# Performance work log

Measured on AMD Instinct MI355X. Metric: run time of the kernel, lower is better.

## Reference

```python
import jax, jax.numpy as jnp
import numpy as np

EPS = 1e-15


def _cdist(a, b):
    # batched euclidean pairwise distance, a:[B,N,K] b:[B,M,K] -> [B,N,M]
    d2 = (jnp.sum(a * a, -1)[:, :, None] + jnp.sum(b * b, -1)[:, None, :]
          - 2.0 * jnp.einsum('bik,bjk->bij', a, b))
    return jnp.sqrt(jnp.maximum(d2, 0.0))


def _rank3_diag(d_flat):
    # [B,N] -> [B,N,N] diagonal
    eye = jnp.eye(d_flat.shape[1], dtype=d_flat.dtype)
    return eye * d_flat[:, :, None]


def _trace(m):
    return jnp.einsum('bjj->b', m)


def dense_ct_rewiring(x, adj, s, mask):
    s = jnp.tanh(s)
    m = mask[:, :, None].astype(x.dtype)
    x = x * m
    s = s * m
    k = s.shape[-1]
    d_flat = jnp.sum(adj, axis=-1)              # [B,N]
    d = _rank3_diag(d_flat) + EPS               # EPS added to full matrix (faithful to torch)
    L = d - adj
    out_adj = jnp.einsum('bnk,bnm,bml->bkl', s, L, s)
    ct_num = _trace(out_adj)
    ct_den = _trace(jnp.einsum('bnk,bnm,bml->bkl', s, d, s)) + EPS
    ct_dist = _cdist(s, s)                      # [B,N,N]
    vol = _trace(d)                             # [B]
    ct_dist = ct_dist / vol[:, None, None]
    adj_new = ct_dist * adj
    ct_loss = jnp.mean(ct_num / ct_den)
    ss = jnp.einsum('bnk,bnl->bkl', s, s)
    i_s = jnp.eye(k, dtype=ss.dtype)
    ss_n = jnp.sqrt(jnp.sum(ss * ss, axis=(-1, -2), keepdims=True))
    diff = ss / ss_n - i_s
    ortho_loss = jnp.sqrt(jnp.sum(diff * diff))  # global Frobenius norm, mean of scalar
    return adj_new, ct_loss, ortho_loss


def dense_mincut_pool(x, adj, s, mask):
    s = jax.nn.softmax(s, axis=-1)
    m = mask[:, :, None].astype(x.dtype)
    x = x * m
    s = s * m
    k = s.shape[-1]
    out = jnp.einsum('bnk,bnf->bkf', s, x)
    out_adj = jnp.einsum('bnk,bnm,bml->bkl', s, adj, s)
    mincut_num = _trace(out_adj)
    d_flat = jnp.sum(adj, axis=-1) + EPS
    d = _rank3_diag(d_flat)
    mincut_den = _trace(jnp.einsum('bnk,bnm,bml->bkl', s, d, s))
    mincut_loss = jnp.mean(-(mincut_num / mincut_den))
    ss = jnp.einsum('bnk,bnl->bkl', s, s)
    i_s = jnp.eye(k, dtype=ss.dtype)
    ss_n = jnp.sqrt(jnp.sum(ss * ss, axis=(-1, -2), keepdims=True))
    diff = ss / ss_n - i_s / jnp.sqrt(jnp.asarray(float(k), ss.dtype))
    ortho_loss = jnp.mean(jnp.sqrt(jnp.sum(diff * diff, axis=(-1, -2))))
    # zero diagonal, then symmetric degree normalization
    out_adj = out_adj * (1.0 - i_s)
    dk = jnp.sqrt(jnp.sum(out_adj, axis=-1) + EPS) + EPS  # [B,k]
    out_adj = out_adj / dk[:, None, :] / dk[:, :, None]
    return out, out_adj, mincut_loss, ortho_loss


def dense_graph_conv(x, adj, w_rel, b_rel, w_root):
    # PyG DenseGraphConv(aggr='add'): lin_rel(adj @ x) + lin_root(x)
    return jnp.matmul(jnp.matmul(adj, x), w_rel) + b_rel + jnp.matmul(x, w_root)


def ctnet_forward(x, adj, mask,
                  W_lin1, b_lin1, W_pool1, b_pool1, W_pool2, b_pool2,
                  Wrel1, brel1, Wroot1, Wrel2, brel2, Wroot2,
                  W_lin2, b_lin2, W_lin3, b_lin3):
    x = jnp.matmul(x, W_lin1) + b_lin1
    s1 = jnp.matmul(x, W_pool1) + b_pool1
    adj, ct_loss, ortho1 = dense_ct_rewiring(x, adj, s1, mask)
    x = dense_graph_conv(x, adj, Wrel1, brel1, Wroot1)
    s2 = jnp.matmul(x, W_pool2) + b_pool2
    x, adj, mincut2, ortho2 = dense_mincut_pool(x, adj, s2, mask)
    x = dense_graph_conv(x, adj, Wrel2, brel2, Wroot2)
    x = jnp.sum(x, axis=1)
    x = jax.nn.relu(jnp.matmul(x, W_lin2) + b_lin2)
    x = jnp.matmul(x, W_lin3) + b_lin3
    return jax.nn.log_softmax(x, axis=-1), ct_loss + ortho1, mincut2 + ortho2


def _init_lin(key, fan_in, fan_out):
    k1, k2 = jax.random.split(key)
    lim = 1.0 / np.sqrt(fan_in)
    W = jax.random.uniform(k1, (fan_in, fan_out), jnp.float32, -lim, lim)
    b = jax.random.uniform(k2, (fan_out,), jnp.float32, -lim, lim)
    return W, b


def setup_inputs() -> dict:
    key = jax.random.key(0)
    ks = jax.random.split(key, 12)
    B, N, Fin, H, K, OUT, K2 = 16, 1024, 128, 32, 64, 10, 16
    x = jax.random.normal(ks[0], (B, N, Fin), jnp.float32)
    adj = jax.random.uniform(ks[1], (B, N, N), jnp.float32)
    mask = jnp.ones((B, N), jnp.bool_)
    W_lin1, b_lin1 = _init_lin(ks[2], Fin, H)
    W_pool1, b_pool1 = _init_lin(ks[3], H, K)
    W_pool2, b_pool2 = _init_lin(ks[4], H, K2)
    Wrel1, brel1 = _init_lin(ks[5], H, H)
    Wroot1, _ = _init_lin(ks[6], H, H)
    Wrel2, brel2 = _init_lin(ks[7], H, H)
    Wroot2, _ = _init_lin(ks[8], H, H)
    W_lin2, b_lin2 = _init_lin(ks[9], H, H)
    W_lin3, b_lin3 = _init_lin(ks[10], H, OUT)
    return dict(x=x, adj=adj, mask=mask,
                W_lin1=W_lin1, b_lin1=b_lin1, W_pool1=W_pool1, b_pool1=b_pool1,
                W_pool2=W_pool2, b_pool2=b_pool2,
                Wrel1=Wrel1, brel1=brel1, Wroot1=Wroot1,
                Wrel2=Wrel2, brel2=brel2, Wroot2=Wroot2,
                W_lin2=W_lin2, b_lin2=b_lin2, W_lin3=W_lin3, b_lin3=b_lin3)


def reference(x, adj, mask,
              W_lin1, b_lin1, W_pool1, b_pool1, W_pool2, b_pool2,
              Wrel1, brel1, Wroot1, Wrel2, brel2, Wroot2,
              W_lin2, b_lin2, W_lin3, b_lin3):
    return ctnet_forward(x, adj, mask,
                         W_lin1, b_lin1, W_pool1, b_pool1, W_pool2, b_pool2,
                         Wrel1, brel1, Wroot1, Wrel2, brel2, Wroot2,
                         W_lin2, b_lin2, W_lin3, b_lin3)
```

## Files before the change

### kernel.cpp

```cpp
#include <hip/hip_runtime.h>

typedef unsigned short u16;
typedef unsigned int   u32;
typedef __attribute__((ext_vector_type(8))) short bf16x8;
typedef __attribute__((ext_vector_type(4))) float f32x4;

#define EPSF 1e-15f

__device__ __forceinline__ float* accp(float* xb, int b, int a) {
    return xb + (size_t)(b*1024 + a/14)*128 + 114 + (a % 14);
}

__device__ __forceinline__ float bf2f(u16 u) {
    union { u32 i; float f; } v; v.i = ((u32)u) << 16; return v.f;
}
__device__ __forceinline__ u16 f2bf(float f) {
    union { u32 i; float f; } v; v.f = f;
    u32 r = v.i + 0x7fffu + ((v.i >> 16) & 1u);
    return (u16)(r >> 16);
}

__global__ __launch_bounds__(256) void k_a(float* xb,
        const float* __restrict__ W1, const float* __restrict__ b1,
        const float* __restrict__ Wp1, const float* __restrict__ bp1)
{
    __shared__ float W1s[128*32];
    __shared__ float Wp1s[32*64];
    __shared__ float xs[16][128];
    __shared__ float x1s[16][32];
    int tid = threadIdx.x;
    for (int i = tid; i < 1024; i += 256)
        *(float4*)&W1s[i*4] = *(const float4*)&W1[i*4];
    for (int i = tid; i < 512; i += 256)
        *(float4*)&Wp1s[i*4] = *(const float4*)&Wp1[i*4];
    int rbase = blockIdx.x*16;
    for (int e = tid; e < 512; e += 256) {
        int rr = e >> 5, c = e & 31;
        *(float4*)&xs[rr][c*4] = *(const float4*)&xb[(size_t)(rbase + rr)*128 + c*4];
    }
    __syncthreads();
    int w = tid >> 6, l = tid & 63;
    int col = l & 31, half = l >> 5;
    #pragma unroll
    for (int i = 0; i < 4; ++i) {
        int rr = w*4 + i;
        float* xr = xb + (size_t)(rbase + rr)*128;
        if (l == 33) xr[96] = 0.f;
        if (l < 15) xr[113 + l] = 0.f;
        float acc = half ? 0.f : b1[col];
        const float* xrow = &xs[rr][half*64];
        const float* wrow = &W1s[half*64*32 + col];
        for (int f = 0; f < 64; ++f) acc += xrow[f]*wrow[f*32];
        acc += __shfl_down(acc, 32);
        if (l < 32) x1s[rr][l] = acc;
    }
    __syncthreads();
    #pragma unroll
    for (int i = 0; i < 4; ++i) {
        int rr = w*4 + i;
        float* xr = xb + (size_t)(rbase + rr)*128;
        if (l < 32) xr[64 + l] = x1s[rr][l];
        float acc = bp1[l];
        for (int h = 0; h < 32; ++h) acc += x1s[rr][h]*Wp1s[h*64 + l];
        float sv = tanhf(acc);
        u32 me = (u32)f2bf(sv);
        u32 nb = __shfl_down(me, 1);
        if (!(l & 1)) ((u32*)xr)[l >> 1] = me | (nb << 16);
        float svr = bf2f((u16)me);
        float qv = svr*svr;
        for (int off = 32; off; off >>= 1) qv += __shfl_down(qv, off);
        if (l == 0) xr[112] = qv;
    }
}

__global__ __launch_bounds__(256, 5) void k_c(const float* __restrict__ adj, float* xb,
                                              u32* __restrict__ anb)
{
    __shared__ __align__(16) u16 BufA[64*72];
    __shared__ __align__(16) u16 BufB[2][64*72];
    __shared__ __align__(16) float qAs[64], qBs[2][64];
    __shared__ float pw[2][4];
    int tid = threadIdx.x;
    int tjq = blockIdx.x, ti = blockIdx.y, b = blockIdx.z;
    int w = tid >> 6, lane = tid & 63;
    int q = lane >> 4, c16 = lane & 15;
    int rloc = w*16 + c16;
    size_t rowg = (size_t)(b*1024 + ti*64 + rloc);
    float4 a4s[2][4];
    #pragma unroll
    for (int tt = 0; tt < 2; ++tt)
        #pragma unroll
        for (int t = 0; t < 4; ++t)
            a4s[tt][t] = *(const float4*)&adj[rowg*1024 + (tjq*2 + tt)*64 + t*16 + q*4];
    const u32* xu = (const u32*)xb;
    for (int e = tid; e < 512; e += 256) {
        int n = e >> 3, c = e & 7;
        *(float4*)&BufA[n*72 + c*8] = *(const float4*)&xu[(size_t)(b*1024 + ti*64 + n)*128 + c*4];
    }
    for (int e = tid; e < 1024; e += 256) {
        int n2 = e >> 3, c = e & 7;
        int tt = n2 >> 6, n = n2 & 63;
        *(float4*)&BufB[tt][n*72 + c*8] =
            *(const float4*)&xu[(size_t)(b*1024 + (tjq*2 + tt)*64 + n)*128 + c*4];
    }
    if (tid < 64) qAs[tid] = xb[(size_t)(b*1024 + ti*64 + tid)*128 + 112];
    else if (tid < 192) {
        int t2 = tid - 64;
        qBs[t2 >> 6][t2 & 63] =
            xb[(size_t)(b*1024 + (tjq*2 + (t2 >> 6))*64 + (t2 & 63))*128 + 112];
    }
    __syncthreads();
    bf16x8 bfr0 = *(const bf16x8*)&BufA[rloc*72 + q*8];
    bf16x8 bfr1 = *(const bf16x8*)&BufA[rloc*72 + 32 + q*8];
    float qa = qAs[rloc];
    float dsum = 0.f, rsum = 0.f, Pt = 0.f, Qt = 0.f;
    #pragma unroll
    for (int tt = 0; tt < 2; ++tt) {
        f32x4 g[4];
        #pragma unroll
        for (int t = 0; t < 4; ++t) {
            bf16x8 af0 = *(const bf16x8*)&BufB[tt][(t*16 + c16)*72 + q*8];
            bf16x8 af1 = *(const bf16x8*)&BufB[tt][(t*16 + c16)*72 + 32 + q*8];
            f32x4 gg = {0.f, 0.f, 0.f, 0.f};
            gg = __builtin_amdgcn_mfma_f32_16x16x32_bf16(af0, bfr0, gg, 0, 0, 0);
            gg = __builtin_amdgcn_mfma_f32_16x16x32_bf16(af1, bfr1, gg, 0, 0, 0);
            g[t] = gg;
        }
        #pragma unroll
        for (int t = 0; t < 4; ++t) {
            float4 a4 = a4s[tt][t];
            float4 qb4 = *(const float4*)&qBs[tt][t*16 + q*4];
            float av[4] = {a4.x, a4.y, a4.z, a4.w};
            float qb[4] = {qb4.x, qb4.y, qb4.z, qb4.w};
            float o[4];
            #pragma unroll
            for (int rg = 0; rg < 4; ++rg) {
                float d2v = qa + qb[rg] - 2.f*g[t][rg];
                float dist = sqrtf(fmaxf(d2v, 0.f));
                o[rg] = dist * av[rg];
                dsum += av[rg];
                rsum += o[rg];
                Pt += av[rg]*g[t][rg];
                Qt += g[t][rg]*g[t][rg];
            }
            u32 p0 = (u32)f2bf(o[0]) | ((u32)f2bf(o[1]) << 16);
            u32 p1 = (u32)f2bf(o[2]) | ((u32)f2bf(o[3]) << 16);
            *(uint2*)&anb[rowg*512 + (tjq*2 + tt)*32 + t*8 + q*2] = make_uint2(p0, p1);
        }
    }
    rsum += __shfl_xor(rsum, 16); rsum += __shfl_xor(rsum, 32);
    dsum += __shfl_xor(dsum, 16); dsum += __shfl_xor(dsum, 32);
    if (q == 0) {
        atomicAdd(&xb[rowg*128 + 96],  dsum);
        atomicAdd(&xb[rowg*128 + 113], rsum);
    }
    for (int off = 32; off; off >>= 1) { Pt += __shfl_down(Pt, off); Qt += __shfl_down(Qt, off); }
    if (lane == 0) { pw[0][w] = Pt; pw[1][w] = Qt; }
    __syncthreads();
    if (tid == 0) {
        atomicAdd(accp(xb,b,3), pw[0][0]+pw[0][1]+pw[0][2]+pw[0][3]);
        atomicAdd(accp(xb,b,4), pw[1][0]+pw[1][1]+pw[1][2]+pw[1][3]);
    }
}

__global__ __launch_bounds__(256) void k_y(const u32* __restrict__ anb, float* xb)
{
    __shared__ __align__(16) u16 X[32][1032];
    int tid = threadIdx.x;
    int ni = blockIdx.x, b = blockIdx.y;
    int w = tid >> 6, lane = tid & 63;
    int q = lane >> 4, c16 = lane & 15;
    int rloc = w*16 + c16;
    size_t rowg = (size_t)(b*1024 + ni*64 + rloc);
    for (int e = tid; e < 8192; e += 256) {
        int m = e >> 3, hq = e & 7;
        const float4 v = *(const float4*)&xb[(size_t)(b*1024 + m)*128 + 64 + hq*4];
        X[hq*4 + 0][m] = f2bf(v.x);
        X[hq*4 + 1][m] = f2bf(v.y);
        X[hq*4 + 2][m] = f2bf(v.z);
        X[hq*4 + 3][m] = f2bf(v.w);
    }
    __syncthreads();
    f32x4 acc0 = {0.f,0.f,0.f,0.f}, acc1 = {0.f,0.f,0.f,0.f};
    #pragma unroll 8
    for (int ks = 0; ks < 32; ++ks) {
        bf16x8 af  = *(const bf16x8*)&anb[rowg*512 + ks*16 + q*4];
        bf16x8 b0  = *(const bf16x8*)&X[c16][ks*32 + q*8];
        bf16x8 b1v = *(const bf16x8*)&X[c16 + 16][ks*32 + q*8];
        acc0 = __builtin_amdgcn_mfma_f32_16x16x32_bf16(af, b0,  acc0, 0, 0, 0);
        acc1 = __builtin_amdgcn_mfma_f32_16x16x32_bf16(af, b1v, acc1, 0, 0, 0);
    }
    #pragma unroll
    for (int rg = 0; rg < 4; ++rg) {
        size_t orow = (size_t)(b*1024 + ni*64 + w*16 + q*4 + rg)*128;
        xb[orow + 32 + c16] = acc0[rg];
        xb[orow + 48 + c16] = acc1[rg];
    }
    if (tid < 64) {
        const float* xr = xb + (size_t)(b*1024 + ni*64 + tid)*128;
        float d = xr[96], qv = xr[112];
        float t0 = d, t1 = d*qv, t2 = qv;
        for (int off = 32; off; off >>= 1) {
            t0 += __shfl_down(t0, off); t1 += __shfl_down(t1, off); t2 += __shfl_down(t2, off);
        }
        if (tid == 0) {
            atomicAdd(accp(xb,b,0), t0);
            atomicAdd(accp(xb,b,1), t1);
            atomicAdd(accp(xb,b,2), t2);
        }
    }
}

__global__ __launch_bounds__(256) void k_d2(float* xb,
        const float* __restrict__ Wrel1, const float* __restrict__ brel1,
        const float* __restrict__ Wroot1,
        const float* __restrict__ Wp2, const float* __restrict__ bp2)
{
    __shared__ float ys[32*34];
    __shared__ float x1n[32*34];
    __shared__ float x2s[32*34];
    __shared__ float s2s[32*17];
    __shared__ float Wr[1024], Wo[1024], Wp[512];
    int tid = threadIdx.x;
    int tq = blockIdx.x, b = blockIdx.y;
    int rbase = b*1024 + tq*32;
    float invv = 1.f / (*accp(xb,b,0) + 1024.f*EPSF);
    for (int i = tid; i < 1024; i += 256) { Wr[i] = Wrel1[i]; Wo[i] = Wroot1[i]; }
    for (int i = tid; i < 512; i += 256) Wp[i] = Wp2[i];
    for (int e = tid; e < 1024; e += 256) {
        int r = e >> 5, h = e & 31;
        const float* xr = xb + (size_t)(rbase + r)*128;
        ys[r*34 + h]  = xr[32 + h] * invv;
        x1n[r*34 + h] = xr[64 + h];
    }
    __syncthreads();
    {
        int h = tid & 31, tg = tid >> 5;
        float brl = brel1[h];
        #pragma unroll
        for (int i = 0; i < 4; ++i) {
            int r = tg + 8*i;
            float v = brl;
            for (int j = 0; j < 32; ++j)
                v += ys[r*34 + j]*Wr[j*32 + h] + x1n[r*34 + j]*Wo[j*32 + h];
            x2s[r*34 + h] = v;
        }
    }
    __syncthreads();
    if (tid < 64) {
        int r = tid & 31;
        float lg[16];
        float mx = -1e30f;
        #pragma unroll
        for (int k = 0; k < 16; ++k) {
            float v = bp2[k];
            for (int j = 0; j < 32; ++j) v += x2s[r*34 + j]*Wp[j*16 + k];
            lg[k] = v; mx = fmaxf(mx, v);
        }
        float sum = 0.f;
        #pragma unroll
        for (int k = 0; k < 16; ++k) { lg[k] = expf(lg[k] - mx); sum += lg[k]; }
        float inv = 1.f/sum, q2v = 0.f;
        u32 pk[8];
        #pragma unroll
        for (int k = 0; k < 16; ++k) {
            float sv = lg[k]*inv;
            s2s[r*17 + k] = sv;
            u32 bfv = (u32)f2bf(sv);
            if (k & 1) pk[k>>1] |= bfv << 16; else pk[k>>1] = bfv;
            q2v += sv*sv;
        }
        if (tid < 32) {
            u32* xp = (u32*)(xb + (size_t)(rbase + r)*128);
            #pragma unroll
            for (int i2 = 0; i2 < 8; ++i2) xp[i2] = pk[i2];
        }
        float denp = (xb[(size_t)(rbase + r)*128 + 113]*invv + EPSF)*q2v;
        if (tid >= 32) denp = 0.f;
        for (int off = 32; off; off >>= 1) denp += __shfl_down(denp, off);
        if (tid == 0) atomicAdd(accp(xb,b,5), denp);
    }
    __syncthreads();
    {
        int k = tid >> 4, l = tid & 15;
        float s = 0.f;
        for (int r = 0; r < 32; ++r) s += s2s[r*17 + k]*s2s[r*17 + l];
        atomicAdd(accp(xb,b,774 + tid), s);
    }
    for (int e = tid; e < 512; e += 256) {
        int k = e >> 5, h = e & 31;
        float s = 0.f;
        for (int r = 0; r < 32; ++r) s += s2s[r*17 + k]*x2s[r*34 + h];
        atomicAdd(accp(xb,b,6 + k*32 + h), s);
    }
}

__global__ __launch_bounds__(256, 6) void k_e(const u32* __restrict__ anb, float* xb)
{
    __shared__ __align__(16) u16 BufA[64*72];
    __shared__ __align__(16) u16 BufS[16*72];
    __shared__ __align__(16) u16 BufN[16*72];
    __shared__ __align__(16) u16 zT[16*72];
    int tid = threadIdx.x;
    int miq = blockIdx.x, ni = blockIdx.y, b = blockIdx.z;
    const u32* xu = (const u32*)xb;
    for (int e = tid; e < 512; e += 256) {
        int node = e >> 3, lw = e & 7;
        u32 pp = xu[(size_t)(b*1024 + ni*64 + node)*128 + lw];
        BufN[(lw*2)*72 + node]     = (u16)pp;
        BufN[(lw*2 + 1)*72 + node] = (u16)(pp >> 16);
    }
    int w = tid >> 6, lane = tid & 63;
    int q = lane >> 4, c16 = lane & 15;
    int rloc = w*16 + c16;
    f32x4 zacc = {0.f, 0.f, 0.f, 0.f};
    #pragma unroll
    for (int mii = 0; mii < 2; ++mii) {
        int mi = miq*2 + mii;
        __syncthreads();
        for (int e = tid; e < 512; e += 256) {
            int n = e >> 3, c = e & 7;
            *(float4*)&BufA[n*72 + c*8] =
                *(const float4*)&anb[(size_t)(b*1024 + ni*64 + n)*512 + mi*32 + c*4];
        }
        for (int e = tid; e < 512; e += 256) {
            int node = e >> 3, lw = e & 7;
            u32 pp = xu[(size_t)(b*1024 + mi*64 + node)*128 + lw];
            BufS[(lw*2)*72 + node]     = (u16)pp;
            BufS[(lw*2 + 1)*72 + node] = (u16)(pp >> 16);
        }
        __syncthreads();
        bf16x8 ya0 = *(const bf16x8*)&BufA[rloc*72 + q*8];
        bf16x8 ya1 = *(const bf16x8*)&BufA[rloc*72 + 32 + q*8];
        bf16x8 yb0 = *(const bf16x8*)&BufS[c16*72 + q*8];
        bf16x8 yb1 = *(const bf16x8*)&BufS[c16*72 + 32 + q*8];
        zacc = __builtin_amdgcn_mfma_f32_16x16x32_bf16(ya0, yb0, zacc, 0, 0, 0);
        zacc = __builtin_amdgcn_mfma_f32_16x16x32_bf16(ya1, yb1, zacc, 0, 0, 0);
    }
    #pragma unroll
    for (int rg = 0; rg < 4; ++rg)
        zT[c16*72 + w*16 + q*4 + rg] = f2bf(zacc[rg]);
    __syncthreads();
    if (w == 0) {
        bf16x8 af0 = *(const bf16x8*)&BufN[c16*72 + q*8];
        bf16x8 af1 = *(const bf16x8*)&BufN[c16*72 + 32 + q*8];
        bf16x8 bz0 = *(const bf16x8*)&zT[c16*72 + q*8];
        bf16x8 bz1 = *(const bf16x8*)&zT[c16*72 + 32 + q*8];
        f32x4 oamv = {0.f, 0.f, 0.f, 0.f};
        oamv = __builtin_amdgcn_mfma_f32_16x16x32_bf16(af0, bz0, oamv, 0, 0, 0);
        oamv = __builtin_amdgcn_mfma_f32_16x16x32_bf16(af1, bz1, oamv, 0, 0, 0);
        #pragma unroll
        for (int rg = 0; rg < 4; ++rg)
            atomicAdd(accp(xb, b, 518 + (q*4 + rg)*16 + c16), oamv[rg]);
    }
}

__global__ __launch_bounds__(256) void k_f1(float* xb,
        const float* __restrict__ Wrel2, const float* __restrict__ brel2,
        const float* __restrict__ Wroot2,
        const float* __restrict__ W_lin2, const float* __restrict__ b_lin2,
        const float* __restrict__ W_lin3, const float* __restrict__ b_lin3,
        float* __restrict__ outp)
{
    __shared__ float oam_s[256], ssm_s[256], outm_s[512];
    __shared__ float dks[16], csoa[16];
    __shared__ float cs0[32], cs1[32], xsum[32], x5[32], lgs[10];
    __shared__ float red[4];
    __shared__ int isLast;
    int b = blockIdx.x;
    int tid = threadIdx.x;
    float invv = 1.f / (*accp(xb,b,0) + 1024.f*EPSF);
    oam_s[tid] = *accp(xb,b,518 + tid) * invv;
    ssm_s[tid] = *accp(xb,b,774 + tid);
    for (int e = tid; e < 512; e += 256) outm_s[e] = *accp(xb,b,6 + e);
    __syncthreads();
    if (tid < 16) {
        float rsv = 0.f;
        for (int l = 0; l < 16; ++l) if (l != tid) rsv += oam_s[tid*16 + l];
        dks[tid] = sqrtf(fmaxf(rsv, 0.f) + EPSF) + EPSF;
    }
    {
        float v = ssm_s[tid];
        float p = v*v;
        for (int off = 32; off; off >>= 1) p += __shfl_down(p, off);
        if ((tid & 63) == 0) red[tid >> 6] = p;
    }
    __syncthreads();
    if (tid < 16) {
        float s = 0.f;
        for (int k2 = 0; k2 < 16; ++k2)
            if (k2 != tid) s += oam_s[k2*16 + tid] / dks[k2];
        csoa[tid] = s / dks[tid];
    }
    if (tid < 32) {
        float s0 = 0.f, s1 = 0.f;
        for (int l = 0; l < 16; ++l) {
            float ov = outm_s[l*32 + tid];
            s0 += ov;
            s1 += csoa[l] * ov;
        }
        cs0[tid] = s0; cs1[tid] = s1;
    }
    if (tid == 64) {
        float T1v  = *accp(xb,b,1);
        float Pgv  = *accp(xb,b,3);
        float Q2v  = *accp(xb,b,4);
        float Tq1v = *accp(xb,b,2);
        float T2v  = *accp(xb,b,5);
        float tr2 = 0.f, trs = 0.f;
        for (int k2 = 0; k2 < 16; ++k2) { tr2 += oam_s[k2*17]; trs += ssm_s[k2*17]; }
        float fr2 = red[0] + red[1] + red[2] + red[3];
        __hip_atomic_store(accp(xb,b,1030), (T1v - Pgv) / (T1v + EPSF),
                           __ATOMIC_RELAXED, __HIP_MEMORY_SCOPE_AGENT);
        __hip_atomic_store(accp(xb,b,1031), 65.f - 2.f*Tq1v/sqrtf(fmaxf(Q2v, 1e-30f)),
                           __ATOMIC_RELAXED, __HIP_MEMORY_SCOPE_AGENT);
        __hip_atomic_store(accp(xb,b,1032), -tr2 / T2v,
                           __ATOMIC_RELAXED, __HIP_MEMORY_SCOPE_AGENT);
        __hip_atomic_store(accp(xb,b,1033),
                           sqrtf(fmaxf(2.f - trs/(2.f*sqrtf(fmaxf(fr2, 1e-30f))), 0.f)),
                           __ATOMIC_RELAXED, __HIP_MEMORY_SCOPE_AGENT);
    }
    __syncthreads();
    if (tid < 32) {
        float v = 16.f * brel2[tid];
        for (int j = 0; j < 32; ++j)
            v += cs1[j]*Wrel2[j*32 + tid] + cs0[j]*Wroot2[j*32 + tid];
        xsum[tid] = v;
    }
    __syncthreads();
    if (tid < 32) {
        float v = b_lin2[tid];
        for (int j = 0; j < 32; ++j) v += xsum[j]*W_lin2[j*32 + tid];
        x5[tid] = fmaxf(v, 0.f);
    }
    __syncthreads();
    if (tid < 10) {
        float v = b_lin3[tid];
        for (int j = 0; j < 32; ++j) v += x5[j]*W_lin3[j*10 + tid];
        lgs[tid] = v;
    }
    __syncthreads();
    if (tid < 10) {
        float mx = -1e30f;
        for (int t = 0; t < 10; ++t) mx = fmaxf(mx, lgs[t]);
        float sum = 0.f;
        for (int t = 0; t < 10; ++t) sum += expf(lgs[t] - mx);
        outp[b*10 + tid] = lgs[tid] - mx - logf(sum);
    }
    __syncthreads();
    if (tid == 0) {
        __threadfence();
        float old = atomicAdd(accp(xb,0,1035), 1.f);
        isLast = (old > 14.5f) ? 1 : 0;
    }
    __syncthreads();
    if (isLast && tid < 64) {
        __threadfence();
        int b2 = tid & 15, which = tid >> 4;
        float v = __hip_atomic_load(accp(xb,b2,1030 + which),
                                    __ATOMIC_RELAXED, __HIP_MEMORY_SCOPE_AGENT);
        for (int off = 1; off < 16; off <<= 1) v += __shfl_xor(v, off);
        float ct = __shfl(v, 0);
        float o1 = __shfl(v, 16);
        float mc = __shfl(v, 32);
        float o2 = __shfl(v, 48);
        if (tid == 0) {
            outp[160] = ct/16.f + sqrtf(fmaxf(o1, 0.f));
            outp[161] = mc/16.f + o2/16.f;
        }
    }
}

extern "C" void kernel_launch(void* const* d_in, const int* in_sizes, int n_in,
                              void* d_out, int out_size, void* d_ws, size_t ws_size,
                              hipStream_t stream)
{
    float* xb        = (float*)d_in[0];
    const float* adj = (const float*)d_in[1];
    const float* W_lin1 = (const float*)d_in[3];
    const float* b_lin1 = (const float*)d_in[4];
    const float* W_pool1= (const float*)d_in[5];
    const float* b_pool1= (const float*)d_in[6];
    const float* W_pool2= (const float*)d_in[7];
    const float* b_pool2= (const float*)d_in[8];
    const float* Wrel1  = (const float*)d_in[9];
    const float* brel1  = (const float*)d_in[10];
    const float* Wroot1 = (const float*)d_in[11];
    const float* Wrel2  = (const float*)d_in[12];
    const float* brel2  = (const float*)d_in[13];
    const float* Wroot2 = (const float*)d_in[14];
    const float* W_lin2 = (const float*)d_in[15];
    const float* b_lin2 = (const float*)d_in[16];
    const float* W_lin3 = (const float*)d_in[17];
    const float* b_lin3 = (const float*)d_in[18];
    u32* anb = (u32*)d_ws;
    (void)ws_size; (void)in_sizes; (void)n_in; (void)out_size;

    k_a<<<dim3(1024),      dim3(256), 0, stream>>>(xb, W_lin1, b_lin1, W_pool1, b_pool1);
    k_c<<<dim3(8,16,16),   dim3(256), 0, stream>>>(adj, xb, anb);
    k_y<<<dim3(16,16),     dim3(256), 0, stream>>>(anb, xb);
    k_d2<<<dim3(32,16),    dim3(256), 0, stream>>>(xb, Wrel1, brel1, Wroot1,
                                                   W_pool2, b_pool2);
    k_e<<<dim3(8,16,16),   dim3(256), 0, stream>>>(anb, xb);
    k_f1<<<dim3(16),       dim3(256), 0, stream>>>(xb, Wrel2, brel2, Wroot2,
                                                   W_lin2, b_lin2, W_lin3, b_lin3,
                                                   (float*)d_out);
}
```

Before: 227.5 us.

## Load MFMA operands directly from global and split k_y across feature halves

In k_c, the per-row A operand and the q value are now loaded straight from global memory into registers instead of being staged through shared memory. This cuts LDS use and lets the occupancy hint rise to 6. In k_e, the adjacency fragments are read directly into registers and both S tiles are staged in one pass, which removes one barrier round. In k_y, the grid is split across two 16-column feature halves, which halves the LDS footprint per block and doubles the block count, but the X transpose is now loaded by both blocks.

Result: slower. 241.8 us (+6.3%).

```diff
diff --git a/kernel.cpp b/kernel.cpp
--- a/kernel.cpp
+++ b/kernel.cpp
@@ -73,12 +73,11 @@
     }
 }
 
-__global__ __launch_bounds__(256, 5) void k_c(const float* __restrict__ adj, float* xb,
+__global__ __launch_bounds__(256, 6) void k_c(const float* __restrict__ adj, float* xb,
                                               u32* __restrict__ anb)
 {
-    __shared__ __align__(16) u16 BufA[64*72];
     __shared__ __align__(16) u16 BufB[2][64*72];
-    __shared__ __align__(16) float qAs[64], qBs[2][64];
+    __shared__ __align__(16) float qBs[2][64];
     __shared__ float pw[2][4];
     int tid = threadIdx.x;
     int tjq = blockIdx.x, ti = blockIdx.y, b = blockIdx.z;
@@ -86,33 +85,27 @@
     int q = lane >> 4, c16 = lane & 15;
     int rloc = w*16 + c16;
     size_t rowg = (size_t)(b*1024 + ti*64 + rloc);
+    const u32* xu = (const u32*)xb;
     float4 a4s[2][4];
     #pragma unroll
     for (int tt = 0; tt < 2; ++tt)
         #pragma unroll
         for (int t = 0; t < 4; ++t)
             a4s[tt][t] = *(const float4*)&adj[rowg*1024 + (tjq*2 + tt)*64 + t*16 + q*4];
-    const u32* xu = (const u32*)xb;
-    for (int e = tid; e < 512; e += 256) {
-        int n = e >> 3, c = e & 7;
-        *(float4*)&BufA[n*72 + c*8] = *(const float4*)&xu[(size_t)(b*1024 + ti*64 + n)*128 + c*4];
-    }
+    bf16x8 bfr0 = *(const bf16x8*)&xu[rowg*128 + q*4];
+    bf16x8 bfr1 = *(const bf16x8*)&xu[rowg*128 + 16 + q*4];
+    float qa = xb[rowg*128 + 112];
     for (int e = tid; e < 1024; e += 256) {
         int n2 = e >> 3, c = e & 7;
         int tt = n2 >> 6, n = n2 & 63;
         *(float4*)&BufB[tt][n*72 + c*8] =
             *(const float4*)&xu[(size_t)(b*1024 + (tjq*2 + tt)*64 + n)*128 + c*4];
     }
-    if (tid < 64) qAs[tid] = xb[(size_t)(b*1024 + ti*64 + tid)*128 + 112];
-    else if (tid < 192) {
-        int t2 = tid - 64;
-        qBs[t2 >> 6][t2 & 63] =
-            xb[(size_t)(b*1024 + (tjq*2 + (t2 >> 6))*64 + (t2 & 63))*128 + 112];
-    }
-    __syncthreads();
-    bf16x8 bfr0 = *(const bf16x8*)&BufA[rloc*72 + q*8];
-    bf16x8 bfr1 = *(const bf16x8*)&BufA[rloc*72 + 32 + q*8];
-    float qa = qAs[rloc];
+    if (tid < 128) {
+        qBs[tid >> 6][tid & 63] =
+            xb[(size_t)(b*1024 + (tjq*2 + (tid >> 6))*64 + (tid & 63))*128 + 112];
+    }
+    __syncthreads();
     float dsum = 0.f, rsum = 0.f, Pt = 0.f, Qt = 0.f;
     #pragma unroll
     for (int tt = 0; tt < 2; ++tt) {
@@ -165,38 +158,39 @@
 
 __global__ __launch_bounds__(256) void k_y(const u32* __restrict__ anb, float* xb)
 {
-    __shared__ __align__(16) u16 X[32][1032];
+    __shared__ __align__(16) u16 X[16*1032];
     int tid = threadIdx.x;
-    int ni = blockIdx.x, b = blockIdx.y;
+    int hq = blockIdx.x, ni = blockIdx.y, b = blockIdx.z;
     int w = tid >> 6, lane = tid & 63;
     int q = lane >> 4, c16 = lane & 15;
     int rloc = w*16 + c16;
     size_t rowg = (size_t)(b*1024 + ni*64 + rloc);
-    for (int e = tid; e < 8192; e += 256) {
-        int m = e >> 3, hq = e & 7;
-        const float4 v = *(const float4*)&xb[(size_t)(b*1024 + m)*128 + 64 + hq*4];
-        X[hq*4 + 0][m] = f2bf(v.x);
-        X[hq*4 + 1][m] = f2bf(v.y);
-        X[hq*4 + 2][m] = f2bf(v.z);
-        X[hq*4 + 3][m] = f2bf(v.w);
-    }
-    __syncthreads();
-    f32x4 acc0 = {0.f,0.f,0.f,0.f}, acc1 = {0.f,0.f,0.f,0.f};
+    u32* Xu = (u32*)X;
+    for (int e = tid; e < 2048; e += 256) {
+        int mp = e >> 2, h4 = e & 3;
+        int m0 = mp*2;
+        const float* p0 = &xb[(size_t)(b*1024 + m0)*128 + 64 + hq*16 + h4*4];
+        float4 v0 = *(const float4*)p0;
+        float4 v1 = *(const float4*)(p0 + 128);
+        Xu[(h4*4 + 0)*516 + mp] = (u32)f2bf(v0.x) | ((u32)f2bf(v1.x) << 16);
+        Xu[(h4*4 + 1)*516 + mp] = (u32)f2bf(v0.y) | ((u32)f2bf(v1.y) << 16);
+        Xu[(h4*4 + 2)*516 + mp] = (u32)f2bf(v0.z) | ((u32)f2bf(v1.z) << 16);
+        Xu[(h4*4 + 3)*516 + mp] = (u32)f2bf(v0.w) | ((u32)f2bf(v1.w) << 16);
+    }
+    __syncthreads();
+    f32x4 acc = {0.f,0.f,0.f,0.f};
     #pragma unroll 8
     for (int ks = 0; ks < 32; ++ks) {
-        bf16x8 af  = *(const bf16x8*)&anb[rowg*512 + ks*16 + q*4];
-        bf16x8 b0  = *(const bf16x8*)&X[c16][ks*32 + q*8];
-        bf16x8 b1v = *(const bf16x8*)&X[c16 + 16][ks*32 + q*8];
-        acc0 = __builtin_amdgcn_mfma_f32_16x16x32_bf16(af, b0,  acc0, 0, 0, 0);
-        acc1 = __builtin_amdgcn_mfma_f32_16x16x32_bf16(af, b1v, acc1, 0, 0, 0);
+        bf16x8 af = *(const bf16x8*)&anb[rowg*512 + ks*16 + q*4];
+        bf16x8 bx = *(const bf16x8*)&X[c16*1032 + ks*32 + q*8];
+        acc = __builtin_amdgcn_mfma_f32_16x16x32_bf16(af, bx, acc, 0, 0, 0);
     }
     #pragma unroll
     for (int rg = 0; rg < 4; ++rg) {
         size_t orow = (size_t)(b*1024 + ni*64 + w*16 + q*4 + rg)*128;
-        xb[orow + 32 + c16] = acc0[rg];
-        xb[orow + 48 + c16] = acc1[rg];
-    }
-    if (tid < 64) {
+        xb[orow + 32 + hq*16 + c16] = acc[rg];
+    }
+    if (hq == 0 && tid < 64) {
         const float* xr = xb + (size_t)(b*1024 + ni*64 + tid)*128;
         float d = xr[96], qv = xr[112];
         float t0 = d, t1 = d*qv, t2 = qv;
@@ -295,10 +289,9 @@
     }
 }
 
-__global__ __launch_bounds__(256, 6) void k_e(const u32* __restrict__ anb, float* xb)
-{
-    __shared__ __align__(16) u16 BufA[64*72];
-    __shared__ __align__(16) u16 BufS[16*72];
+__global__ __launch_bounds__(256) void k_e(const u32* __restrict__ anb, float* xb)
+{
+    __shared__ __align__(16) u16 BufS[2][16*72];
     __shared__ __align__(16) u16 BufN[16*72];
     __shared__ __align__(16) u16 zT[16*72];
     int tid = threadIdx.x;
@@ -310,32 +303,31 @@
         BufN[(lw*2)*72 + node]     = (u16)pp;
         BufN[(lw*2 + 1)*72 + node] = (u16)(pp >> 16);
     }
+    for (int e = tid; e < 1024; e += 256) {
+        int t = e >> 9, e2 = e & 511;
+        int node = e2 >> 3, lw = e2 & 7;
+        u32 pp = xu[(size_t)(b*1024 + (miq*2 + t)*64 + node)*128 + lw];
+        BufS[t][(lw*2)*72 + node]     = (u16)pp;
+        BufS[t][(lw*2 + 1)*72 + node] = (u16)(pp >> 16);
+    }
     int w = tid >> 6, lane = tid & 63;
     int q = lane >> 4, c16 = lane & 15;
     int rloc = w*16 + c16;
+    size_t arow = (size_t)(b*1024 + ni*64 + rloc)*512;
+    bf16x8 ya[2][2];
+    #pragma unroll
+    for (int t = 0; t < 2; ++t) {
+        ya[t][0] = *(const bf16x8*)&anb[arow + (miq*2 + t)*32 + q*4];
+        ya[t][1] = *(const bf16x8*)&anb[arow + (miq*2 + t)*32 + 16 + q*4];
+    }
+    __syncthreads();
     f32x4 zacc = {0.f, 0.f, 0.f, 0.f};
     #pragma unroll
-    for (int mii = 0; mii < 2; ++mii) {
-        int mi = miq*2 + mii;
-        __syncthreads();
-        for (int e = tid; e < 512; e += 256) {
-            int n = e >> 3, c = e & 7;
-            *(float4*)&BufA[n*72 + c*8] =
-                *(const float4*)&anb[(size_t)(b*1024 + ni*64 + n)*512 + mi*32 + c*4];
-        }
-        for (int e = tid; e < 512; e += 256) {
-            int node = e >> 3, lw = e & 7;
-            u32 pp = xu[(size_t)(b*1024 + mi*64 + node)*128 + lw];
-            BufS[(lw*2)*72 + node]     = (u16)pp;
-            BufS[(lw*2 + 1)*72 + node] = (u16)(pp >> 16);
-        }
-        __syncthreads();
-        bf16x8 ya0 = *(const bf16x8*)&BufA[rloc*72 + q*8];
-        bf16x8 ya1 = *(const bf16x8*)&BufA[rloc*72 + 32 + q*8];
-        bf16x8 yb0 = *(const bf16x8*)&BufS[c16*72 + q*8];
-        bf16x8 yb1 = *(const bf16x8*)&BufS[c16*72 + 32 + q*8];
-        zacc = __builtin_amdgcn_mfma_f32_16x16x32_bf16(ya0, yb0, zacc, 0, 0, 0);
-        zacc = __builtin_amdgcn_mfma_f32_16x16x32_bf16(ya1, yb1, zacc, 0, 0, 0);
+    for (int t = 0; t < 2; ++t) {
+        bf16x8 yb0 = *(const bf16x8*)&BufS[t][c16*72 + q*8];
+        bf16x8 yb1 = *(const bf16x8*)&BufS[t][c16*72 + 32 + q*8];
+        zacc = __builtin_amdgcn_mfma_f32_16x16x32_bf16(ya[t][0], yb0, zacc, 0, 0, 0);
+        zacc = __builtin_amdgcn_mfma_f32_16x16x32_bf16(ya[t][1], yb1, zacc, 0, 0, 0);
     }
     #pragma unroll
     for (int rg = 0; rg < 4; ++rg)
@@ -498,7 +490,7 @@
 
     k_a<<<dim3(1024),      dim3(256), 0, stream>>>(xb, W_lin1, b_lin1, W_pool1, b_pool1);
     k_c<<<dim3(8,16,16),   dim3(256), 0, stream>>>(adj, xb, anb);
-    k_y<<<dim3(16,16),     dim3(256), 0, stream>>>(anb, xb);
+    k_y<<<dim3(2,16,16),   dim3(256), 0, stream>>>(anb, xb);
     k_d2<<<dim3(32,16),    dim3(256), 0, stream>>>(xb, Wrel1, brel1, Wroot1,
                                                    W_pool2, b_pool2);
     k_e<<<dim3(8,16,16),   dim3(256), 0, stream>>>(anb, xb);
```
